# Kernel optimization log

Measured on AMD Instinct MI355X. Metric: run time of the kernel, lower is better.

Reference implementation:

```python
import jax, jax.numpy as jnp
import numpy as np

IN_C, OUT_C, K, G, STRIDE = 16, 16, 3, 64, 1
B, H, W = 16, 512, 512


def setup_inputs() -> dict:
    key = jax.random.key(0)
    k1, k2, k3 = jax.random.split(key, 3)
    x = jax.random.normal(k1, (B, IN_C, H, W), dtype=jnp.float32)
    spectral_params = jax.random.normal(k2, (K * IN_C, K * OUT_C), dtype=jnp.float32)
    attn_w = jax.random.normal(k3, (G, IN_C), dtype=jnp.float32) * 0.1  # 1x1 conv weight
    attn_b = jnp.zeros((G,), dtype=jnp.float32)                          # 1x1 conv bias
    return {"x": x, "spectral_params": spectral_params, "attn_w": attn_w, "attn_b": attn_b}


def _group_map():
    # radial frequency index over the [K*IN_C, K*OUT_C] spectral grid
    gi = jnp.linspace(-0.5, 0.5, K * IN_C)
    gj = jnp.linspace(-0.5, 0.5, K * OUT_C)
    idx = jnp.sqrt(gi[:, None] ** 2 + gj[None, :] ** 2)
    thresholds = jnp.linspace(0.0, 0.5, G + 1)
    # bucket i satisfies thresholds[i] <= idx < thresholds[i+1]
    gid = jnp.searchsorted(thresholds, idx, side='right') - 1
    valid = (idx < 0.5) & (gid >= 0) & (gid < G)
    return jnp.where(valid, gid, 0), valid


def reference(x, spectral_params, attn_w, attn_b):
    b, c, h, w = x.shape
    gid, valid = _group_map()  # [KC, KO] int, [KC, KO] bool
    # attention gate: global avg pool -> 1x1 conv -> sigmoid  -> [b, G]
    pooled = x.mean(axis=(2, 3))                              # [b, c]
    pi = jax.nn.sigmoid(pooled @ attn_w.T + attn_b)           # [b, G]
    # group masks are disjoint radial bands, so the mixture collapses to a
    # per-element gather of the gate value (0 outside all bands)
    gate = jnp.where(valid[None], pi[:, gid], 0.0)            # [b, KC, KO]
    dyn = spectral_params[None] * gate                        # [b, KC, KO]
    # view(in, k, out, k).permute(2,0,1,3) -> [b, out, in, k, k]
    dyn = dyn.reshape(b, IN_C, K, OUT_C, K).transpose(0, 3, 1, 2, 4)
    kernel = dyn.reshape(b * OUT_C, IN_C, K, K)
    # per-sample dynamic conv as a single grouped conv (groups = batch)
    out = jax.lax.conv_general_dilated(
        x.reshape(1, b * c, h, w), kernel,
        window_strides=(STRIDE, STRIDE), padding='VALID',
        dimension_numbers=('NCHW', 'OIHW', 'NCHW'),
        feature_group_count=b)
    return out.reshape(b, OUT_C, out.shape[2], out.shape[3])
```

## Files before the change

kernel.cpp:

```cpp
#include <hip/hip_runtime.h>


#define BATCH 16
#define CH 16
#define HIN 512
#define WIN 512
#define HOUT 510
#define WOUT 510

typedef _Float16 half8 __attribute__((ext_vector_type(8)));
typedef float f32x4 __attribute__((ext_vector_type(4)));


__global__ __launch_bounds__(256) void transform_kernel(const float* __restrict__ x,
                                                        unsigned short* __restrict__ xt,
                                                        float* __restrict__ psum) {
    const int blk = blockIdx.x;
    const int b = blk >> 8, within = blk & 255;
    const int tid = threadIdx.x;
    const int p0 = (within * 256 + tid) * 4;
    const float* xb = x + ((size_t)b << 22);

    f32x4 v[16];
    float s[16];
#pragma unroll
    for (int c = 0; c < 16; ++c) {
        v[c] = __builtin_nontemporal_load((const f32x4*)(xb + ((size_t)c << 18) + p0));
        s[c] = (v[c][0] + v[c][1]) + (v[c][2] + v[c][3]);
    }

    union { _Float16 h[64]; uint4 q[8]; } u;
#pragma unroll
    for (int c = 0; c < 16; ++c) {
        u.h[0 * 16 + c] = (_Float16)v[c][0];
        u.h[1 * 16 + c] = (_Float16)v[c][1];
        u.h[2 * 16 + c] = (_Float16)v[c][2];
        u.h[3 * 16 + c] = (_Float16)v[c][3];
    }
    uint4* dst = (uint4*)(xt + ((size_t)((b << 18) + p0)) * 16);
#pragma unroll
    for (int k = 0; k < 8; ++k) dst[k] = u.q[k];

#pragma unroll
    for (int c = 0; c < 16; ++c) {
        float r = s[c];
        r += __shfl_xor(r, 1);  r += __shfl_xor(r, 2);  r += __shfl_xor(r, 4);
        r += __shfl_xor(r, 8);  r += __shfl_xor(r, 16); r += __shfl_xor(r, 32);
        s[c] = r;
    }
    if ((tid & 63) == 0) {
        float* ps = psum + (size_t)(b * 1024 + within * 4 + (tid >> 6)) * 16;
#pragma unroll
        for (int c = 0; c < 16; ++c) ps[c] = s[c];
    }
}

__global__ __launch_bounds__(256) void stage2_kernel(const float* __restrict__ psum,
                                                     const float* __restrict__ attn_w,
                                                     const float* __restrict__ attn_b,
                                                     const float* __restrict__ spectral,
                                                     unsigned short* __restrict__ wpack) {
    const int b = blockIdx.x, t = threadIdx.x;
    const int c = t & 15, m = t >> 4;
    float s = 0.f;
    for (int j = 0; j < 64; ++j) s += psum[((size_t)b * 1024 + m + j * 16) * 16 + c];
    __shared__ float red[256];
    __shared__ float pooled[16];
    __shared__ float pis[64];
    red[t] = s;
    __syncthreads();
    for (int off = 8; off; off >>= 1) {
        if (m < off) red[t] += red[t + off * 16];
        __syncthreads();
    }
    if (t < 16) pooled[t] = red[t] * (1.f / 262144.f);
    __syncthreads();
    if (t < 64) {
        float a = attn_b[t];
#pragma unroll
        for (int c2 = 0; c2 < 16; ++c2) a += pooled[c2] * attn_w[t * 16 + c2];
        pis[t] = 1.f / (1.f + expf(-a));
    }
    __syncthreads();
    for (int e = t; e < 320; e += 256) {
        const int c5 = e >> 6, lane = e & 63;
        const int o = lane & 15, g = lane >> 4;
        union { _Float16 h[8]; uint4 q; } u;
#pragma unroll
        for (int j = 0; j < 8; ++j) {
            const int kap = c5 * 32 + g * 8 + j;
            const int tp = kap >> 4, i = kap & 15;
            float wv = 0.f;
            if (tp < 9) {
                const int ki = tp / 3, kj = tp - ki * 3;
                const int r = i * 3 + ki, cc = o * 3 + kj;
                const float gi = -0.5f + (float)r * (1.f / 47.f);
                const float gj = -0.5f + (float)cc * (1.f / 47.f);
                const float d2 = gi * gi + gj * gj;
                if (d2 < 0.25f) {
                    int gid = (int)(sqrtf(d2) * 128.f);
                    gid = gid < 63 ? gid : 63;
                    wv = spectral[r * 48 + cc] * pis[gid];
                }
            }
            u.h[j] = (_Float16)wv;
        }
        *(uint4*)(wpack + ((size_t)(b * 5 + c5) * 64 + lane) * 8) = u.q;
    }
}

#define PITCH 4224
__global__ __launch_bounds__(512) void conv_mfma_kernel(const unsigned short* __restrict__ xt,
                                                        const unsigned short* __restrict__ wpack,
                                                        float* __restrict__ out) {
    const int b = blockIdx.y;
    const int cg = blockIdx.x & 3;
    const int yg = blockIdx.x >> 2;
    const int tid = threadIdx.x;
    const int lane = tid & 63, wv = tid >> 6;
    const int y0 = yg * 8, x0g = cg * 128;

    __shared__ unsigned char lds[10 * PITCH];

    half8 wf[5];
    {
        const uint4* wp = (const uint4*)wpack + (size_t)b * 5 * 64 + lane;
#pragma unroll
        for (int c5 = 0; c5 < 5; ++c5) wf[c5] = __builtin_bit_cast(half8, wp[c5 * 64]);
    }

    for (int e = tid; e < 2600; e += 512) {
        const int rr = e / 260;
        const int rem = e - rr * 260;
        const int p = rem >> 1, h = rem & 1;
        int ir = y0 + rr;  ir = ir < 511 ? ir : 511;
        int ic = x0g + p;  ic = ic < 511 ? ic : 511;
        const uint4 v = *(const uint4*)(xt + ((((size_t)b << 18) + (ir << 9) + ic) << 4) + h * 8);
        unsigned a = (unsigned)(rr * PITCH + p * 32 + h * 16);
        a ^= (a >> 3) & 0x30u;
        *(uint4*)(lds + a) = v;
    }
    __syncthreads();

    const int n = lane & 15, g = lane >> 4;
    const int y = y0 + wv;

    unsigned base[5];
#pragma unroll
    for (int c5 = 0; c5 < 5; ++c5) {
        const int tp = 2 * c5 + (g >> 1);
        unsigned a;
        if (tp == 9) {
            a = 0;
        } else {
            const int dy = tp / 3, dx = tp - dy * 3;
            a = (unsigned)((wv + dy) * PITCH + (n + dx) * 32 + (g & 1) * 16);
            a ^= (a >> 3) & 0x30u;
        }
        base[c5] = a;
    }

    const bool ymask = (y < HOUT);
    float* dst0 = out + ((size_t)(b * 16 + n) * HOUT + y) * WOUT + x0g + g * 4;

#pragma unroll
    for (int tt = 0; tt < 8; ++tt) {
        half8 xf[5];
#pragma unroll
        for (int c5 = 0; c5 < 5; ++c5)
            xf[c5] = __builtin_bit_cast(half8, *(const uint4*)(lds + (base[c5] + tt * 512)));
        f32x4 acc = {0.f, 0.f, 0.f, 0.f};
#pragma unroll
        for (int c5 = 0; c5 < 5; ++c5)
            acc = __builtin_amdgcn_mfma_f32_16x16x32_f16(xf[c5], wf[c5], acc, 0, 0, 0);
        if (ymask) {
            const int pb = x0g + tt * 16 + g * 4;
            float* dst = dst0 + tt * 16;
            if (pb + 3 < WOUT) {
                ((float2*)dst)[0] = make_float2(acc[0], acc[1]);
                ((float2*)dst)[1] = make_float2(acc[2], acc[3]);
            } else {
#pragma unroll
                for (int r = 0; r < 4; ++r)
                    if (pb + r < WOUT) dst[r] = acc[r];
            }
        }
    }
}

#define TW 128
#define TH 8
#define XW 132

__global__ __launch_bounds__(256) void pool_kernel(const float* __restrict__ x,
                                                   float* __restrict__ pooled) {
    const int bc = blockIdx.x;
    const float4* src = (const float4*)(x + ((size_t)bc << 18));
    float s = 0.f;
    for (int e = threadIdx.x; e < (HIN * WIN / 4); e += 256) {
        float4 v = src[e];
        s += (v.x + v.y) + (v.z + v.w);
    }
    __shared__ float red[256];
    red[threadIdx.x] = s;
    __syncthreads();
    for (int off = 128; off > 0; off >>= 1) {
        if (threadIdx.x < off) red[threadIdx.x] += red[threadIdx.x + off];
        __syncthreads();
    }
    if (threadIdx.x == 0) pooled[bc] = red[0] * (1.0f / (HIN * WIN));
}

__global__ __launch_bounds__(256) void attn_kernel(const float* __restrict__ pooled,
                                                   const float* __restrict__ attn_w,
                                                   const float* __restrict__ attn_b,
                                                   float* __restrict__ pi) {
    int t = blockIdx.x * 256 + threadIdx.x;
    if (t >= BATCH * 64) return;
    int b = t >> 6, g = t & 63;
    float s = attn_b[g];
#pragma unroll
    for (int c = 0; c < CH; ++c) s += pooled[b * CH + c] * attn_w[g * CH + c];
    pi[t] = 1.0f / (1.0f + expf(-s));
}

__global__ __launch_bounds__(256) void weight_kernel(const float* __restrict__ spectral,
                                                     const float* __restrict__ pi,
                                                     float* __restrict__ wbuf) {
    int idx = blockIdx.x * 256 + threadIdx.x;
    if (idx >= BATCH * CH * CH * 12) return;
    int tap = idx % 12;
    int o = (idx / 12) % CH;
    int i = (idx / 192) % CH;
    int b = idx / 3072;
    float w = 0.f;
    if (tap < 9) {
        int ki = tap / 3, kj = tap % 3;
        int r = i * 3 + ki, c = o * 3 + kj;
        float gi = -0.5f + (float)r * (1.0f / 47.0f);
        float gj = -0.5f + (float)c * (1.0f / 47.0f);
        float d2 = gi * gi + gj * gj;
        if (d2 < 0.25f) {
            int gid = (int)(sqrtf(d2) * 128.0f);
            gid = gid < 63 ? gid : 63;
            w = spectral[r * 48 + c] * pi[b * 64 + gid];
        }
    }
    wbuf[idx] = w;
}

__global__ __launch_bounds__(256) void conv_kernel(const float* __restrict__ x,
                                                   const float* __restrict__ wbuf,
                                                   float* __restrict__ out) {
    const int b = blockIdx.y;
    const int tc = blockIdx.x & 3;
    const int tr = blockIdx.x >> 2;
    __shared__ float xs[10 * XW];
    __shared__ float ws[CH * CH * 12];
    {
        const float4* src = (const float4*)(wbuf + (size_t)b * (CH * CH * 12));
        float4* dst = (float4*)ws;
        for (int e = threadIdx.x; e < 768; e += 256) dst[e] = src[e];
    }
    const int r0 = tr * TH, c0 = tc * TW;
    const int px = (threadIdx.x & 31) * 4, py = threadIdx.x >> 5;
    float acc[16][4];
#pragma unroll
    for (int o = 0; o < 16; ++o)
#pragma unroll
        for (int p = 0; p < 4; ++p) acc[o][p] = 0.f;
    for (int i = 0; i < CH; ++i) {
        __syncthreads();
        const float* xsrc = x + (((size_t)b * CH + i) << 18);
        for (int e = threadIdx.x; e < 330; e += 256) {
            int rr = e / 33;
            int c4 = (e - rr * 33) * 4;
            int ir = r0 + rr, ic = c0 + c4;
            float4 v;
            if (ir < HIN && ic + 3 < WIN) {
                v = *(const float4*)(xsrc + ((size_t)ir << 9) + ic);
            } else {
                v.x = v.y = v.z = v.w = 0.f;
                if (ir < HIN) {
                    const float* row = xsrc + ((size_t)ir << 9);
                    if (ic + 0 < WIN) v.x = row[ic + 0];
                    if (ic + 1 < WIN) v.y = row[ic + 1];
                    if (ic + 2 < WIN) v.z = row[ic + 2];
                    if (ic + 3 < WIN) v.w = row[ic + 3];
                }
            }
            *(float4*)(xs + rr * XW + c4) = v;
        }
        __syncthreads();
        float xv[3][8];
#pragma unroll
        for (int kr = 0; kr < 3; ++kr) {
            float4 a = *(const float4*)(xs + (py + kr) * XW + px);
            float4 c = *(const float4*)(xs + (py + kr) * XW + px + 4);
            xv[kr][0] = a.x; xv[kr][1] = a.y; xv[kr][2] = a.z; xv[kr][3] = a.w;
            xv[kr][4] = c.x; xv[kr][5] = c.y; xv[kr][6] = c.z; xv[kr][7] = c.w;
        }
#pragma unroll
        for (int o = 0; o < 16; ++o) {
            const float* wrow = ws + (i * 16 + o) * 12;
            float4 w0 = *(const float4*)wrow;
            float4 w1 = *(const float4*)(wrow + 4);
            float w8 = wrow[8];
#pragma unroll
            for (int p = 0; p < 4; ++p) {
                float s = acc[o][p];
                s += xv[0][p + 0] * w0.x;
                s += xv[0][p + 1] * w0.y;
                s += xv[0][p + 2] * w0.z;
                s += xv[1][p + 0] * w0.w;
                s += xv[1][p + 1] * w1.x;
                s += xv[1][p + 2] * w1.y;
                s += xv[2][p + 0] * w1.z;
                s += xv[2][p + 1] * w1.w;
                s += xv[2][p + 2] * w8;
                acc[o][p] = s;
            }
        }
    }
    const int oy = r0 + py, ox = c0 + px;
    if (oy < HOUT) {
#pragma unroll
        for (int o = 0; o < 16; ++o) {
            float* orow = out + (((size_t)(b * 16 + o)) * HOUT + oy) * WOUT + ox;
            if (ox + 3 < WOUT) {
                ((float2*)orow)[0] = make_float2(acc[o][0], acc[o][1]);
                ((float2*)orow)[1] = make_float2(acc[o][2], acc[o][3]);
            } else {
#pragma unroll
                for (int p = 0; p < 4; ++p)
                    if (ox + p < WOUT) orow[p] = acc[o][p];
            }
        }
    }
}

extern "C" void kernel_launch(void* const* d_in, const int* in_sizes, int n_in,
                              void* d_out, int out_size, void* d_ws, size_t ws_size,
                              hipStream_t stream) {
    const float* x = (const float*)d_in[0];
    const float* spectral = (const float*)d_in[1];
    const float* attn_w = (const float*)d_in[2];
    const float* attn_b = (const float*)d_in[3];
    float* out = (float*)d_out;

    const size_t XT_BYTES = (size_t)16 * 512 * 512 * 16 * 2;
    const size_t PSUM_BYTES = (size_t)16 * 1024 * 16 * 4;
    const size_t WPACK_BYTES = (size_t)16 * 5 * 64 * 8 * 2;
    const size_t NEED = XT_BYTES + PSUM_BYTES + WPACK_BYTES;

    if (ws_size >= NEED) {
        unsigned short* xt = (unsigned short*)d_ws;
        float* psum = (float*)((char*)d_ws + XT_BYTES);
        unsigned short* wpack = (unsigned short*)((char*)d_ws + XT_BYTES + PSUM_BYTES);

        transform_kernel<<<dim3(4096), dim3(256), 0, stream>>>(x, xt, psum);
        stage2_kernel<<<dim3(16), dim3(256), 0, stream>>>(psum, attn_w, attn_b, spectral, wpack);
        conv_mfma_kernel<<<dim3(256, 16), dim3(512), 0, stream>>>(xt, wpack, out);
    } else {
        float* ws = (float*)d_ws;
        float* pooled = ws;
        float* pi = ws + 256;
        float* wbuf = ws + 1280;
        pool_kernel<<<dim3(BATCH * CH), dim3(256), 0, stream>>>(x, pooled);
        attn_kernel<<<dim3(4), dim3(256), 0, stream>>>(pooled, attn_w, attn_b, pi);
        weight_kernel<<<dim3((BATCH * CH * CH * 12 + 255) / 256), dim3(256), 0, stream>>>(spectral, pi, wbuf);
        conv_kernel<<<dim3(4 * 64, BATCH), dim3(256), 0, stream>>>(x, wbuf, out);
    }
}
```

Baseline: 212.6 us.

## Load conv input fragments directly from global memory instead of LDS staging

```diff
diff --git a/kernel.cpp b/kernel.cpp
--- a/kernel.cpp
+++ b/kernel.cpp
@@ -109,18 +109,17 @@
     }
 }
 
-#define PITCH 4224
-__global__ __launch_bounds__(512) void conv_mfma_kernel(const unsigned short* __restrict__ xt,
-                                                        const unsigned short* __restrict__ wpack,
-                                                        float* __restrict__ out) {
+__global__ __launch_bounds__(512, 4) void conv_mfma_kernel(const unsigned short* __restrict__ xt,
+                                                           const unsigned short* __restrict__ wpack,
+                                                           float* __restrict__ out) {
     const int b = blockIdx.y;
     const int cg = blockIdx.x & 3;
     const int yg = blockIdx.x >> 2;
     const int tid = threadIdx.x;
     const int lane = tid & 63, wv = tid >> 6;
     const int y0 = yg * 8, x0g = cg * 128;
-
-    __shared__ unsigned char lds[10 * PITCH];
+    const int n = lane & 15, g = lane >> 4;
+    const int y = y0 + wv;
 
     half8 wf[5];
     {
@@ -129,35 +128,18 @@
         for (int c5 = 0; c5 < 5; ++c5) wf[c5] = __builtin_bit_cast(half8, wp[c5 * 64]);
     }
 
-    for (int e = tid; e < 2600; e += 512) {
-        const int rr = e / 260;
-        const int rem = e - rr * 260;
-        const int p = rem >> 1, h = rem & 1;
-        int ir = y0 + rr;  ir = ir < 511 ? ir : 511;
-        int ic = x0g + p;  ic = ic < 511 ? ic : 511;
-        const uint4 v = *(const uint4*)(xt + ((((size_t)b << 18) + (ir << 9) + ic) << 4) + h * 8);
-        unsigned a = (unsigned)(rr * PITCH + p * 32 + h * 16);
-        a ^= (a >> 3) & 0x30u;
-        *(uint4*)(lds + a) = v;
-    }
-    __syncthreads();
-
-    const int n = lane & 15, g = lane >> 4;
-    const int y = y0 + wv;
-
-    unsigned base[5];
+    const uint4* xq = (const uint4*)xt + ((size_t)b << 19);
+    const uint4* src[5];
+    int colb[5];
 #pragma unroll
     for (int c5 = 0; c5 < 5; ++c5) {
         const int tp = 2 * c5 + (g >> 1);
-        unsigned a;
-        if (tp == 9) {
-            a = 0;
-        } else {
-            const int dy = tp / 3, dx = tp - dy * 3;
-            a = (unsigned)((wv + dy) * PITCH + (n + dx) * 32 + (g & 1) * 16);
-            a ^= (a >> 3) & 0x30u;
-        }
-        base[c5] = a;
+        int dy, dx;
+        if (tp >= 9) { dy = 0; dx = 0; }
+        else         { dy = tp / 3; dx = tp - 3 * dy; }
+        int ry = y + dy;  ry = ry < 511 ? ry : 511;
+        src[c5] = xq + ((size_t)ry << 10) + (g & 1);
+        colb[c5] = x0g + n + dx;
     }
 
     const bool ymask = (y < HOUT);
@@ -167,8 +149,11 @@
     for (int tt = 0; tt < 8; ++tt) {
         half8 xf[5];
 #pragma unroll
-        for (int c5 = 0; c5 < 5; ++c5)
-            xf[c5] = __builtin_bit_cast(half8, *(const uint4*)(lds + (base[c5] + tt * 512)));
+        for (int c5 = 0; c5 < 5; ++c5) {
+            int col = colb[c5] + tt * 16;
+            col = col < 511 ? col : 511;
+            xf[c5] = __builtin_bit_cast(half8, src[c5][(size_t)col << 1]);
+        }
         f32x4 acc = {0.f, 0.f, 0.f, 0.f};
 #pragma unroll
         for (int c5 = 0; c5 < 5; ++c5)
```

New measurement: 300.3 us. 1.41x slower.

## Make conv blocks persistent over four row tiles with register-staged prefetch

Applied to the files above, without the earlier changes.

```diff
diff --git a/kernel.cpp b/kernel.cpp
--- a/kernel.cpp
+++ b/kernel.cpp
@@ -113,12 +113,16 @@
 __global__ __launch_bounds__(512) void conv_mfma_kernel(const unsigned short* __restrict__ xt,
                                                         const unsigned short* __restrict__ wpack,
                                                         float* __restrict__ out) {
-    const int b = blockIdx.y;
-    const int cg = blockIdx.x & 3;
-    const int yg = blockIdx.x >> 2;
+    const int bid = blockIdx.x;
+    const int g4 = bid & 15;
+    const int cg = (bid >> 4) & 3;
+    const int b = bid >> 6;
+    const int x0g = cg * 128;
+    const int ygBase = g4 * 4;
+
     const int tid = threadIdx.x;
     const int lane = tid & 63, wv = tid >> 6;
-    const int y0 = yg * 8, x0g = cg * 128;
+    const int n = lane & 15, g = lane >> 4;
 
     __shared__ unsigned char lds[10 * PITCH];
 
@@ -129,21 +133,24 @@
         for (int c5 = 0; c5 < 5; ++c5) wf[c5] = __builtin_bit_cast(half8, wp[c5 * 64]);
     }
 
-    for (int e = tid; e < 2600; e += 512) {
-        const int rr = e / 260;
-        const int rem = e - rr * 260;
+    int s_rr[6];
+    int s_ic[6];
+    unsigned s_lda[6];
+    bool s_ok[6];
+#pragma unroll
+    for (int k = 0; k < 6; ++k) {
+        const int e = tid + k * 512;
+        const bool ok = (e < 2600);
+        const int ee = ok ? e : 0;
+        const int rr = ee / 260;
+        const int rem = ee - rr * 260;
         const int p = rem >> 1, h = rem & 1;
-        int ir = y0 + rr;  ir = ir < 511 ? ir : 511;
         int ic = x0g + p;  ic = ic < 511 ? ic : 511;
-        const uint4 v = *(const uint4*)(xt + ((((size_t)b << 18) + (ir << 9) + ic) << 4) + h * 8);
         unsigned a = (unsigned)(rr * PITCH + p * 32 + h * 16);
         a ^= (a >> 3) & 0x30u;
-        *(uint4*)(lds + a) = v;
-    }
-    __syncthreads();
-
-    const int n = lane & 15, g = lane >> 4;
-    const int y = y0 + wv;
+        s_rr[k] = rr;  s_ic[k] = ic * 2 + h;  s_lda[k] = a;  s_ok[k] = ok;
+    }
+    const uint4* xb = (const uint4*)xt + ((size_t)b << 19);
 
     unsigned base[5];
 #pragma unroll
@@ -160,30 +167,66 @@
         base[c5] = a;
     }
 
-    const bool ymask = (y < HOUT);
-    float* dst0 = out + ((size_t)(b * 16 + n) * HOUT + y) * WOUT + x0g + g * 4;
-
-#pragma unroll
-    for (int tt = 0; tt < 8; ++tt) {
-        half8 xf[5];
-#pragma unroll
-        for (int c5 = 0; c5 < 5; ++c5)
-            xf[c5] = __builtin_bit_cast(half8, *(const uint4*)(lds + (base[c5] + tt * 512)));
-        f32x4 acc = {0.f, 0.f, 0.f, 0.f};
-#pragma unroll
-        for (int c5 = 0; c5 < 5; ++c5)
-            acc = __builtin_amdgcn_mfma_f32_16x16x32_f16(xf[c5], wf[c5], acc, 0, 0, 0);
-        if (ymask) {
-            const int pb = x0g + tt * 16 + g * 4;
-            float* dst = dst0 + tt * 16;
-            if (pb + 3 < WOUT) {
-                ((float2*)dst)[0] = make_float2(acc[0], acc[1]);
-                ((float2*)dst)[1] = make_float2(acc[2], acc[3]);
-            } else {
-#pragma unroll
-                for (int r = 0; r < 4; ++r)
-                    if (pb + r < WOUT) dst[r] = acc[r];
-            }
+    uint4 stg[6];
+
+    {
+        const int y0 = ygBase * 8;
+#pragma unroll
+        for (int k = 0; k < 6; ++k) {
+            int ir = y0 + s_rr[k];  ir = ir < 511 ? ir : 511;
+            if (s_ok[k]) stg[k] = xb[((size_t)ir << 10) + s_ic[k]];
+        }
+#pragma unroll
+        for (int k = 0; k < 6; ++k)
+            if (s_ok[k]) *(uint4*)(lds + s_lda[k]) = stg[k];
+    }
+    __syncthreads();
+
+    for (int t = 0; t < 4; ++t) {
+        const int y0 = (ygBase + t) * 8;
+        const int y = y0 + wv;
+
+        if (t < 3) {
+            const int ny0 = y0 + 8;
+#pragma unroll
+            for (int k = 0; k < 6; ++k) {
+                int ir = ny0 + s_rr[k];  ir = ir < 511 ? ir : 511;
+                if (s_ok[k]) stg[k] = xb[((size_t)ir << 10) + s_ic[k]];
+            }
+        }
+
+        const bool ymask = (y < HOUT);
+        float* dst0 = out + ((size_t)(b * 16 + n) * HOUT + y) * WOUT + x0g + g * 4;
+#pragma unroll
+        for (int tt = 0; tt < 8; ++tt) {
+            half8 xf[5];
+#pragma unroll
+            for (int c5 = 0; c5 < 5; ++c5)
+                xf[c5] = __builtin_bit_cast(half8, *(const uint4*)(lds + (base[c5] + tt * 512)));
+            f32x4 acc = {0.f, 0.f, 0.f, 0.f};
+#pragma unroll
+            for (int c5 = 0; c5 < 5; ++c5)
+                acc = __builtin_amdgcn_mfma_f32_16x16x32_f16(xf[c5], wf[c5], acc, 0, 0, 0);
+            if (ymask) {
+                const int pb = x0g + tt * 16 + g * 4;
+                float* dst = dst0 + tt * 16;
+                if (pb + 3 < WOUT) {
+                    ((float2*)dst)[0] = make_float2(acc[0], acc[1]);
+                    ((float2*)dst)[1] = make_float2(acc[2], acc[3]);
+                } else {
+#pragma unroll
+                    for (int r = 0; r < 4; ++r)
+                        if (pb + r < WOUT) dst[r] = acc[r];
+                }
+            }
+        }
+
+        if (t < 3) {
+            __syncthreads();
+#pragma unroll
+            for (int k = 0; k < 6; ++k)
+                if (s_ok[k]) *(uint4*)(lds + s_lda[k]) = stg[k];
+            __syncthreads();
         }
     }
 }
@@ -360,7 +403,7 @@
 
         transform_kernel<<<dim3(4096), dim3(256), 0, stream>>>(x, xt, psum);
         stage2_kernel<<<dim3(16), dim3(256), 0, stream>>>(psum, attn_w, attn_b, spectral, wpack);
-        conv_mfma_kernel<<<dim3(256, 16), dim3(512), 0, stream>>>(xt, wpack, out);
+        conv_mfma_kernel<<<dim3(1024), dim3(512), 0, stream>>>(xt, wpack, out);
     } else {
         float* ws = (float*)d_ws;
         float* pooled = ws;
```

New measurement: 256.0 us. 1.2x slower.

## Retile dynamic conv blocks to two full-width output rows with contiguous LDS staging

Applied to the files above, without the earlier changes.

```diff
diff --git a/kernel.cpp b/kernel.cpp
--- a/kernel.cpp
+++ b/kernel.cpp
@@ -109,18 +109,20 @@
     }
 }
 
-#define PITCH 4224
+#define ROWP 16384
 __global__ __launch_bounds__(512) void conv_mfma_kernel(const unsigned short* __restrict__ xt,
                                                         const unsigned short* __restrict__ wpack,
                                                         float* __restrict__ out) {
     const int b = blockIdx.y;
-    const int cg = blockIdx.x & 3;
-    const int yg = blockIdx.x >> 2;
+    const int y0 = blockIdx.x * 2;
+
     const int tid = threadIdx.x;
     const int lane = tid & 63, wv = tid >> 6;
-    const int y0 = yg * 8, x0g = cg * 128;
-
-    __shared__ unsigned char lds[10 * PITCH];
+    const int n = lane & 15, g = lane >> 4;
+    const int cg = wv & 3, rw = wv >> 2;
+    const int y = y0 + rw;
+
+    __shared__ unsigned char lds[4 * ROWP];
 
     half8 wf[5];
     {
@@ -129,61 +131,57 @@
         for (int c5 = 0; c5 < 5; ++c5) wf[c5] = __builtin_bit_cast(half8, wp[c5 * 64]);
     }
 
-    for (int e = tid; e < 2600; e += 512) {
-        const int rr = e / 260;
-        const int rem = e - rr * 260;
-        const int p = rem >> 1, h = rem & 1;
-        int ir = y0 + rr;  ir = ir < 511 ? ir : 511;
-        int ic = x0g + p;  ic = ic < 511 ? ic : 511;
-        const uint4 v = *(const uint4*)(xt + ((((size_t)b << 18) + (ir << 9) + ic) << 4) + h * 8);
-        unsigned a = (unsigned)(rr * PITCH + p * 32 + h * 16);
-        a ^= (a >> 3) & 0x30u;
-        *(uint4*)(lds + a) = v;
-    }
-    __syncthreads();
-
-    const int n = lane & 15, g = lane >> 4;
-    const int y = y0 + wv;
-
-    unsigned base[5];
+    {
+        const uint4* xb = (const uint4*)xt + ((size_t)b << 19);
+#pragma unroll
+        for (int k = 0; k < 8; ++k) {
+            const int e = tid + k * 512;
+            const int rr = e >> 10, q = e & 1023;
+            const uint4 v = xb[((size_t)(y0 + rr) << 10) + q];
+            unsigned a = (unsigned)(e << 4);
+            a ^= (a >> 3) & 0x30u;
+            *(uint4*)(lds + a) = v;
+        }
+    }
+    __syncthreads();
+
+    unsigned q0[5], rb[5];
 #pragma unroll
     for (int c5 = 0; c5 < 5; ++c5) {
         const int tp = 2 * c5 + (g >> 1);
-        unsigned a;
         if (tp == 9) {
-            a = 0;
+            q0[c5] = 0; rb[c5] = 0;
         } else {
             const int dy = tp / 3, dx = tp - dy * 3;
-            a = (unsigned)((wv + dy) * PITCH + (n + dx) * 32 + (g & 1) * 16);
-            a ^= (a >> 3) & 0x30u;
-        }
-        base[c5] = a;
-    }
-
-    const bool ymask = (y < HOUT);
-    float* dst0 = out + ((size_t)(b * 16 + n) * HOUT + y) * WOUT + x0g + g * 4;
+            q0[c5] = (unsigned)((cg * 128 + n + dx) * 32 + (g & 1) * 16);
+            rb[c5] = (unsigned)((rw + dy) * ROWP);
+        }
+    }
+
+    float* dst0 = out + ((size_t)(b * 16 + n) * HOUT + y) * WOUT + cg * 128 + g * 4;
 
 #pragma unroll
     for (int tt = 0; tt < 8; ++tt) {
         half8 xf[5];
 #pragma unroll
-        for (int c5 = 0; c5 < 5; ++c5)
-            xf[c5] = __builtin_bit_cast(half8, *(const uint4*)(lds + (base[c5] + tt * 512)));
+        for (int c5 = 0; c5 < 5; ++c5) {
+            unsigned a = (q0[c5] + tt * 512u) & 16383u;
+            a ^= (a >> 3) & 0x30u;
+            xf[c5] = __builtin_bit_cast(half8, *(const uint4*)(lds + (rb[c5] + a)));
+        }
         f32x4 acc = {0.f, 0.f, 0.f, 0.f};
 #pragma unroll
         for (int c5 = 0; c5 < 5; ++c5)
             acc = __builtin_amdgcn_mfma_f32_16x16x32_f16(xf[c5], wf[c5], acc, 0, 0, 0);
-        if (ymask) {
-            const int pb = x0g + tt * 16 + g * 4;
-            float* dst = dst0 + tt * 16;
-            if (pb + 3 < WOUT) {
-                ((float2*)dst)[0] = make_float2(acc[0], acc[1]);
-                ((float2*)dst)[1] = make_float2(acc[2], acc[3]);
-            } else {
-#pragma unroll
-                for (int r = 0; r < 4; ++r)
-                    if (pb + r < WOUT) dst[r] = acc[r];
-            }
+        const int pb = cg * 128 + tt * 16 + g * 4;
+        float* dst = dst0 + tt * 16;
+        if (pb + 3 < WOUT) {
+            ((float2*)dst)[0] = make_float2(acc[0], acc[1]);
+            ((float2*)dst)[1] = make_float2(acc[2], acc[3]);
+        } else {
+#pragma unroll
+            for (int r = 0; r < 4; ++r)
+                if (pb + r < WOUT) dst[r] = acc[r];
         }
     }
 }
@@ -360,7 +358,7 @@
 
         transform_kernel<<<dim3(4096), dim3(256), 0, stream>>>(x, xt, psum);
         stage2_kernel<<<dim3(16), dim3(256), 0, stream>>>(psum, attn_w, attn_b, spectral, wpack);
-        conv_mfma_kernel<<<dim3(256, 16), dim3(512), 0, stream>>>(xt, wpack, out);
+        conv_mfma_kernel<<<dim3(255, 16), dim3(512), 0, stream>>>(xt, wpack, out);
     } else {
         float* ws = (float*)d_ws;
         float* pooled = ws;
```

After: 199.2 us. -6.3%, faster.
